# Performance work log

Hardware: AMD Instinct MI355X
Metric: run time of the kernel (lower is better)

Reference implementation:

```python
import jax, jax.numpy as jnp
import numpy as np

# SSD Detect post-processing constants (match init_kwargs)
NUM_CLASSES = 21
TOP_K = 200
CONF_THRESH = 0.95
NMS_THRESH = 0.45
M_CAND = 600      # candidate cap; chosen so all boxes passing CONF_THRESH fit (~437 expected)
NEG = -1e30


def setup_inputs() -> dict:
    key = jax.random.key(0)
    k1, k2, k3 = jax.random.split(key, 3)
    B, P, C = 8, 8732, NUM_CLASSES
    loc_data = jax.random.normal(k1, (B, P, 4), dtype=jnp.float32)
    conf_data = jax.random.uniform(k2, (B, P, C), dtype=jnp.float32)
    prior_data = jax.random.uniform(k3, (1, P, 4), dtype=jnp.float32)
    return {"loc_data": loc_data, "conf_data": conf_data, "prior_data": prior_data}


def _nms_lane(boxes_all, scores):
    """One (batch, class) lane. boxes_all: [P,4], scores: [P]. Returns [TOP_K, 5]."""
    pass_mask = scores > CONF_THRESH                       # [P]
    masked = jnp.where(pass_mask, scores, jnp.float32(NEG))
    vals, idx = jax.lax.top_k(masked, M_CAND)              # score-desc candidates (prior idx)
    valid = vals > jnp.float32(NEG / 2)                    # passed threshold
    cb = boxes_all[idx]                                    # [M,4] (x1,y1,x2,y2)
    x1, y1, x2, y2 = cb[:, 0], cb[:, 1], cb[:, 2], cb[:, 3]
    area = (x2 - x1) * (y2 - y1)                           # torchvision-style, no clamp
    xx1 = jnp.maximum(x1[:, None], x1[None, :])
    yy1 = jnp.maximum(y1[:, None], y1[None, :])
    xx2 = jnp.minimum(x2[:, None], x2[None, :])
    yy2 = jnp.minimum(y2[:, None], y2[None, :])
    inter = jnp.clip(xx2 - xx1, 0.0) * jnp.clip(yy2 - yy1, 0.0)
    iou = inter / (area[:, None] + area[None, :] - inter)  # [M,M]
    ar = jnp.arange(M_CAND)

    def body(i, supp):
        keep_i = valid[i] & jnp.logical_not(supp[i])
        return supp | (keep_i & (iou[i] > NMS_THRESH) & (ar > i))

    supp = jax.lax.fori_loop(0, M_CAND, body, jnp.zeros((M_CAND,), bool))
    keep = valid & jnp.logical_not(supp)
    order = jnp.argsort(jnp.logical_not(keep))             # stable: kept first, score order
    n = jnp.minimum(keep.sum(), TOP_K)                     # number of kept boxes (<= TOP_K)
    sel_prior = idx[order[:TOP_K]]                         # prior ids of kept (score order)
    slot_valid = jnp.arange(TOP_K) < n
    fp = jnp.argmax(pass_mask)                             # first prior passing threshold
    prior_ids = jnp.where(slot_valid, sel_prior, fp)       # pad with boxes[0] like torch
    out_scores = jnp.where(slot_valid, scores[prior_ids], 0.0)
    out = jnp.concatenate([out_scores[:, None], boxes_all[prior_ids]], axis=1)  # [K,5]
    return jnp.where(pass_mask.any(), out, jnp.zeros_like(out))


def _forward(loc_data, conf_data, prior_data):
    # prior_data is accepted per the torch signature but unused by the forward math.
    per_batch = jax.vmap(
        lambda boxes, conf_b: jax.vmap(lambda s: _nms_lane(boxes, s))(conf_b[:, 1:].T)
    )
    out_fg = per_batch(loc_data, conf_data)                # [B, C-1, K, 5]
    bg = jnp.zeros_like(out_fg[:, :1])                     # background class row stays 0
    return jnp.concatenate([bg, out_fg], axis=1)           # [B, C, K, 5]


def reference(loc_data, conf_data, prior_data):
    return _forward(loc_data, conf_data, prior_data)
```

## Files before the change

### kernel.cpp

```cpp
#include <hip/hip_runtime.h>
#include <float.h>
#include <math.h>


#define P_PRIORS  8732
#define C_CLASSES 21
#define B_BATCH   8
#define TOPK      200
#define MCAND     600
#define CONF_T    0.95f
#define NMS_T     0.45f
#define NB        64
#define MINB      0x3F733334u

__device__ __forceinline__ uint64_t pack_key(float sc, int p) {
    return ((uint64_t)__float_as_uint(sc) << 32) | (uint32_t)(~(uint32_t)p);
}
__device__ __forceinline__ int bucket_of(uint64_t key) {
    unsigned d = (unsigned)(key >> 32) - MINB;
    int b = (int)(d >> 14);
    return b < (NB - 1) ? b : (NB - 1);
}

#define IOU_ROW(BI, AI, MW, DIAG) do {                                   \
    float xx1 = fmaxf((BI).x, bj.x);                                     \
    float yy1 = fmaxf((BI).y, bj.y);                                     \
    float xx2 = fminf((BI).z, bj.z);                                     \
    float yy2 = fminf((BI).w, bj.w);                                     \
    float ww  = fmaxf(xx2 - xx1, 0.0f);                                  \
    float hh  = fmaxf(yy2 - yy1, 0.0f);                                  \
    float inter = ww * hh;                                               \
    float den   = ((AI) + aj) - inter;              \
    float iou   = inter / den;               \
    uint64_t m = __ballot(iou > NMS_T);                                  \
    if (k == c) m &= (DIAG);                                             \
    (MW) = (lid == k) ? m : (MW);                                        \
} while (0)

__device__ __forceinline__ void iou_chunk(
    int c, int wid, int lid, int M, int kend,
    const float4* s_jb, const float* s_area, uint64_t* s_bm)
{
    const int i0 = (c << 6) + wid;
    const float4 b0 = s_jb[i0],      b1 = s_jb[i0 + 16],
                 b2 = s_jb[i0 + 32], b3 = s_jb[i0 + 48];
    const float  a0 = s_area[i0],      a1 = s_area[i0 + 16],
                 a2 = s_area[i0 + 32], a3 = s_area[i0 + 48];
    const uint64_t d0 = ~0ull << (wid + 1);
    const uint64_t d1 = ~0ull << (wid + 17);
    const uint64_t d2 = ~0ull << (wid + 33);
    const uint64_t d3 = (wid == 15) ? 0ull : (~0ull << (wid + 49));
    uint64_t w0 = 0, w1 = 0, w2 = 0, w3 = 0;
    for (int k = c; k < kend; ++k) {
        const float4 bj = s_jb[(k << 6) + lid];
        const float  aj = s_area[(k << 6) + lid];
        IOU_ROW(b0, a0, w0, d0);
        IOU_ROW(b1, a1, w1, d1);
        IOU_ROW(b2, a2, w2, d2);
        IOU_ROW(b3, a3, w3, d3);
    }
    if (lid >= c && lid < kend) {
        if (i0      < M) s_bm[(size_t)(i0     ) * 10 + lid] = w0;
        if (i0 + 16 < M) s_bm[(size_t)(i0 + 16) * 10 + lid] = w1;
        if (i0 + 32 < M) s_bm[(size_t)(i0 + 32) * 10 + lid] = w2;
        if (i0 + 48 < M) s_bm[(size_t)(i0 + 48) * 10 + lid] = w3;
    }
}

__global__ __launch_bounds__(1024) void detect_one(
    const float* __restrict__ loc, const float* __restrict__ conf,
    float* __restrict__ out)
{
    const int b   = blockIdx.x & 7;
    const int cls = blockIdx.x >> 3;
    const int tid = threadIdx.x;
    float* o = out + ((size_t)(b * C_CLASSES + cls)) * TOPK * 5;

    if (cls == 0) {
        for (int k = tid; k < TOPK * 5; k += 1024) o[k] = 0.0f;
        return;
    }

    const float*  confb = conf + (size_t)b * P_PRIORS * C_CLASSES + cls;
    const float4* loc4  = (const float4*)(loc + (size_t)b * P_PRIORS * 4);

    __shared__ uint64_t s_bm[MCAND * 10];
    __shared__ float4   s_jb[640];
    __shared__ float    s_area[640];
    __shared__ float    s_ssc[MCAND];
    __shared__ int      s_bcnt[NB], s_bcur[NB], s_boff[NB];
    __shared__ int      s_cnt, s_fp;
    __shared__ uint64_t s_suppw[10], s_keepw[10];
    __shared__ int      s_prefix[10], s_n, s_mstop, s_done;

    uint64_t* s_k   = s_bm;
    uint64_t* s_g   = s_bm + 1024;
    uint64_t* s_srt = s_bm + 2048;

    if (tid < NB)                    s_bcnt[tid] = 0;
    else if (tid < 2 * NB)           s_bcur[tid - NB] = 0;
    else if (tid == 2 * NB)        { s_cnt = 0; s_fp = 0x7FFFFFFF; }
    __syncthreads();

    {
        const int lid = tid & 63;
        float vcur  = confb[(size_t)tid * C_CLASSES];
        float vnext = confb[(size_t)(tid + 1024) * C_CLASSES];
        #pragma unroll
        for (int r = 0; r < 9; ++r) {
            float v = vcur;
            vcur = vnext;
            if (r + 2 <= 7) {
                vnext = confb[(size_t)(tid + ((r + 2) << 10)) * C_CLASSES];
            } else if (r + 2 == 8) {
                int pn = tid + 8192;
                vnext = (pn < P_PRIORS) ? confb[(size_t)pn * C_CLASSES] : 0.0f;
            } else {
                vnext = 0.0f;
            }
            int p = tid + (r << 10);
            bool pass = v > CONF_T;
            uint64_t mask = __ballot(pass);
            if (mask != 0) {
                int leader = (int)__ffsll((unsigned long long)mask) - 1;
                int base = 0;
                if (lid == leader) {
                    base = atomicAdd(&s_cnt, __popcll(mask));
                    atomicMin(&s_fp, p);
                }
                base = __shfl(base, leader, 64);
                if (pass) {
                    int pos = base + __popcll(mask & ((1ull << lid) - 1ull));
                    if (pos < 1024) s_k[pos] = pack_key(v, p);
                }
            }
        }
    }
    __syncthreads();
    int cnt = s_cnt; if (cnt > 1024) cnt = 1024;
    if (cnt == 0) {
        for (int k = tid; k < TOPK * 5; k += 1024) o[k] = 0.0f;
        return;
    }

    for (int t = tid; t < cnt; t += 1024)
        atomicAdd(&s_bcnt[bucket_of(s_k[t])], 1);
    __syncthreads();

    if (tid < 64) {
        int c = s_bcnt[63 - tid];
        int incl = c;
        #pragma unroll
        for (int d = 1; d < 64; d <<= 1) {
            int u = __shfl_up(incl, d, 64);
            if (tid >= d) incl += u;
        }
        s_boff[63 - tid] = incl - c;
    }
    __syncthreads();

    for (int t = tid; t < cnt; t += 1024) {
        uint64_t kt = s_k[t];
        int bb = bucket_of(kt);
        s_g[s_boff[bb] + atomicAdd(&s_bcur[bb], 1)] = kt;
    }
    __syncthreads();

    const int M = cnt < MCAND ? cnt : MCAND;
    {
        const int wid = tid >> 6, lid = tid & 63;
        for (int bb = wid; bb < NB; bb += 16) {
            int st = s_boff[bb], n = s_bcnt[bb];
            for (int e = lid; e < n; e += 64) {
                uint64_t kq = s_g[st + e];
                int r = st;
                for (int q = 0; q < n; ++q)
                    r += (s_g[st + q] > kq) ? 1 : 0;
                if (r < MCAND) s_srt[r] = kq;
            }
        }
    }
    __syncthreads();

    for (int i = tid; i < M; i += 1024) {
        uint64_t key = s_srt[i];
        int p = (int)(~(uint32_t)key);
        s_ssc[i]  = __uint_as_float((uint32_t)(key >> 32));
        float4 bx = loc4[p];
        s_jb[i]   = bx;
        s_area[i] = (bx.z - bx.x) * (bx.w - bx.y);
    }
    for (int i = M + tid; i < 640; i += 1024) {
        s_jb[i]   = make_float4(INFINITY, INFINITY, INFINITY, INFINITY);
        s_area[i] = INFINITY;
    }
    const int fp = s_fp;
    __syncthreads();

    const int kmax = (M + 63) >> 6;
    const int kcap = kmax < 5 ? kmax : 5;

    {
        const int wid = tid >> 6, lid = tid & 63;
        const int w   = (lid < 10) ? lid : 0;
        uint64_t supp = 0;
        int kept = 0, mstop = M;
        const int nch = kcap;

        iou_chunk(0, wid, lid, M, kcap, s_jb, s_area, s_bm);
        __syncthreads();

        for (int c = 0; c < nch; ++c) {
            if (wid == 0) {
                const int ibeg = c << 6;
                const int iend = min(ibeg + 64, M);
                uint64_t rb[8];
                #pragma unroll
                for (int d = 0; d < 8; ++d) {
                    int i = ibeg + d;
                    rb[d] = (i < iend) ? s_bm[(size_t)i * 10 + w] : 0;
                }
                for (int i = ibeg; i < iend; ++i) {
                    uint64_t row = rb[i & 7];
                    if (w < c) row = 0;
                    int ip = i + 8;
                    rb[i & 7] = (ip < iend) ? s_bm[(size_t)ip * 10 + w] : 0;
                    bool mybit = (w == c) && ((supp >> (i & 63)) & 1ull);
                    if (!__any((int)mybit)) {
                        supp |= row;
                        if (++kept == TOPK) { mstop = i + 1; break; }
                    }
                }
                if (lid == 0) s_done = (kept >= TOPK) ? 1 : 0;
                if (kept < TOPK && c + 1 < nch)
                    iou_chunk(c + 1, 0, lid, M, kcap, s_jb, s_area, s_bm);
            } else if (c + 1 < nch) {
                iou_chunk(c + 1, wid, lid, M, kcap, s_jb, s_area, s_bm);
            }
            __syncthreads();
            if (s_done) break;
        }
        if (wid == 0) {
            if (lid < 10) s_suppw[lid] = supp;
            if (lid == 0) s_mstop = mstop;
        }
    }
    __syncthreads();

    if (s_done == 0 && M > 320) {
        const int wid = tid >> 6, lid = tid & 63;
        for (int i = wid; i < M; i += 16) {
            float4 bi = s_jb[i];
            float  ai = s_area[i];
            const int k0 = i >> 6;
            uint64_t diag = ((i & 63) == 63) ? 0ull : (~0ull << ((i & 63) + 1));
            uint64_t myw = 0;
            for (int k = k0; k < kmax; ++k) {
                float4 bj = s_jb[(k << 6) + lid];
                float  aj = s_area[(k << 6) + lid];
                float xx1 = fmaxf(bi.x, bj.x);
                float yy1 = fmaxf(bi.y, bj.y);
                float xx2 = fminf(bi.z, bj.z);
                float yy2 = fminf(bi.w, bj.w);
                float ww  = fmaxf(xx2 - xx1, 0.0f);
                float hh  = fmaxf(yy2 - yy1, 0.0f);
                float inter = ww * hh;
                float den   = (ai + aj) - inter;
                float iou   = inter / den;
                uint64_t m = __ballot(iou > NMS_T);
                if (k == k0) m &= diag;
                myw = (lid == k) ? m : myw;
            }
            if (lid >= k0 && lid < kmax) s_bm[(size_t)i * 10 + lid] = myw;
        }
        __syncthreads();
        if (tid < 64) {
            const int w = (tid < 10) ? tid : 0;
            uint64_t supp = 0;
            int kept = 0, ms = M;
            for (int i = 0; i < M; ++i) {
                uint64_t row = s_bm[(size_t)i * 10 + w];
                if (w < (i >> 6)) row = 0;
                unsigned part  = (unsigned)(supp >> (i & 32));
                unsigned wordv = (unsigned)__builtin_amdgcn_readlane((int)part, i >> 6);
                if (!((wordv >> (i & 31)) & 1u)) {
                    supp |= row;
                    if (++kept == TOPK) { ms = i + 1; break; }
                }
            }
            if (tid < 10) s_suppw[tid] = supp;
            if (tid == 0) s_mstop = ms;
        }
        __syncthreads();
    }

    if (tid == 0) {
        const int Me = s_mstop;
        int total = 0;
        for (int w = 0; w < 10; ++w) {
            uint64_t kw = 0;
            int rem = Me - (w << 6);
            if (rem > 0) {
                uint64_t vm = (rem >= 64) ? ~0ull : ((1ull << rem) - 1ull);
                kw = (~s_suppw[w]) & vm;
            }
            s_keepw[w]  = kw;
            s_prefix[w] = total;
            total += __popcll(kw);
        }
        s_n = total < TOPK ? total : TOPK;
    }
    __syncthreads();

    const int n  = s_n;
    const int Me = s_mstop;
    float4 fbox = loc4[fp];
    for (int k = tid; k < TOPK; k += 1024) {
        if (k >= n) {
            o[k * 5 + 0] = 0.0f;
            o[k * 5 + 1] = fbox.x; o[k * 5 + 2] = fbox.y;
            o[k * 5 + 3] = fbox.z; o[k * 5 + 4] = fbox.w;
        }
    }
    for (int t = tid; t < Me; t += 1024) {
        uint64_t kw = s_keepw[t >> 6];
        if ((kw >> (t & 63)) & 1ull) {
            int r = s_prefix[t >> 6] + __popcll(kw & ((1ull << (t & 63)) - 1ull));
            if (r < TOPK) {
                float4 bx = s_jb[t];
                o[r * 5 + 0] = s_ssc[t];
                o[r * 5 + 1] = bx.x; o[r * 5 + 2] = bx.y;
                o[r * 5 + 3] = bx.z; o[r * 5 + 4] = bx.w;
            }
        }
    }
}

extern "C" void kernel_launch(void* const* d_in, const int* in_sizes, int n_in,
                              void* d_out, int out_size, void* d_ws, size_t ws_size,
                              hipStream_t stream) {
    const float* loc  = (const float*)d_in[0];
    const float* conf = (const float*)d_in[1];
    float* out = (float*)d_out;
    (void)d_ws; (void)ws_size;

    detect_one<<<dim3(B_BATCH * C_CLASSES), dim3(1024), 0, stream>>>(loc, conf, out);
}
```

Before: 105.0 us.

## Replace bucketed rank sort with flat rank sort and prefetch IoU column boxes

Drops the 64-bucket histogram, scan and scatter stages and instead ranks each candidate key by comparing it against all candidates in a single O(n^2) pass over shared memory. This removes two barriers and the atomic bucket passes in exchange for more comparisons per thread (about 437 reads each, all threads reading the same address, which is a broadcast). It also software-pipelines the IoU chunk loop by loading the next column's box and area before computing the current rows, to hide LDS latency.

Measured after the change: 109.7 us. 4.5% more time.

```diff
diff --git a/kernel.cpp b/kernel.cpp
--- a/kernel.cpp
+++ b/kernel.cpp
@@ -10,16 +10,9 @@
 #define MCAND     600
 #define CONF_T    0.95f
 #define NMS_T     0.45f
-#define NB        64
-#define MINB      0x3F733334u
 
 __device__ __forceinline__ uint64_t pack_key(float sc, int p) {
     return ((uint64_t)__float_as_uint(sc) << 32) | (uint32_t)(~(uint32_t)p);
-}
-__device__ __forceinline__ int bucket_of(uint64_t key) {
-    unsigned d = (unsigned)(key >> 32) - MINB;
-    int b = (int)(d >> 14);
-    return b < (NB - 1) ? b : (NB - 1);
 }
 
 #define IOU_ROW(BI, AI, MW, DIAG) do {                                   \
@@ -51,13 +44,19 @@
     const uint64_t d2 = ~0ull << (wid + 33);
     const uint64_t d3 = (wid == 15) ? 0ull : (~0ull << (wid + 49));
     uint64_t w0 = 0, w1 = 0, w2 = 0, w3 = 0;
+    float4 bj = s_jb[(c << 6) + lid];
+    float  aj = s_area[(c << 6) + lid];
     for (int k = c; k < kend; ++k) {
-        const float4 bj = s_jb[(k << 6) + lid];
-        const float  aj = s_area[(k << 6) + lid];
+        float4 bjn = bj; float ajn = aj;
+        if (k + 1 < kend) {
+            bjn = s_jb[((k + 1) << 6) + lid];
+            ajn = s_area[((k + 1) << 6) + lid];
+        }
         IOU_ROW(b0, a0, w0, d0);
         IOU_ROW(b1, a1, w1, d1);
         IOU_ROW(b2, a2, w2, d2);
         IOU_ROW(b3, a3, w3, d3);
+        bj = bjn; aj = ajn;
     }
     if (lid >= c && lid < kend) {
         if (i0      < M) s_bm[(size_t)(i0     ) * 10 + lid] = w0;
@@ -88,18 +87,14 @@
     __shared__ float4   s_jb[640];
     __shared__ float    s_area[640];
     __shared__ float    s_ssc[MCAND];
-    __shared__ int      s_bcnt[NB], s_bcur[NB], s_boff[NB];
     __shared__ int      s_cnt, s_fp;
     __shared__ uint64_t s_suppw[10], s_keepw[10];
     __shared__ int      s_prefix[10], s_n, s_mstop, s_done;
 
     uint64_t* s_k   = s_bm;
-    uint64_t* s_g   = s_bm + 1024;
     uint64_t* s_srt = s_bm + 2048;
 
-    if (tid < NB)                    s_bcnt[tid] = 0;
-    else if (tid < 2 * NB)           s_bcur[tid - NB] = 0;
-    else if (tid == 2 * NB)        { s_cnt = 0; s_fp = 0x7FFFFFFF; }
+    if (tid == 0) { s_cnt = 0; s_fp = 0x7FFFFFFF; }
     __syncthreads();
 
     {
@@ -143,45 +138,16 @@
         return;
     }
 
-    for (int t = tid; t < cnt; t += 1024)
-        atomicAdd(&s_bcnt[bucket_of(s_k[t])], 1);
-    __syncthreads();
-
-    if (tid < 64) {
-        int c = s_bcnt[63 - tid];
-        int incl = c;
-        #pragma unroll
-        for (int d = 1; d < 64; d <<= 1) {
-            int u = __shfl_up(incl, d, 64);
-            if (tid >= d) incl += u;
-        }
-        s_boff[63 - tid] = incl - c;
-    }
-    __syncthreads();
-
     for (int t = tid; t < cnt; t += 1024) {
         uint64_t kt = s_k[t];
-        int bb = bucket_of(kt);
-        s_g[s_boff[bb] + atomicAdd(&s_bcur[bb], 1)] = kt;
+        int r = 0;
+        for (int q = 0; q < cnt; ++q)
+            r += (s_k[q] > kt) ? 1 : 0;
+        if (r < MCAND) s_srt[r] = kt;
     }
     __syncthreads();
 
     const int M = cnt < MCAND ? cnt : MCAND;
-    {
-        const int wid = tid >> 6, lid = tid & 63;
-        for (int bb = wid; bb < NB; bb += 16) {
-            int st = s_boff[bb], n = s_bcnt[bb];
-            for (int e = lid; e < n; e += 64) {
-                uint64_t kq = s_g[st + e];
-                int r = st;
-                for (int q = 0; q < n; ++q)
-                    r += (s_g[st + q] > kq) ? 1 : 0;
-                if (r < MCAND) s_srt[r] = kq;
-            }
-        }
-    }
-    __syncthreads();
-
     for (int i = tid; i < M; i += 1024) {
         uint64_t key = s_srt[i];
         int p = (int)(~(uint32_t)key);
```

## Offload next-chunk IoU rows from the NMS-scan wave to the other 15 waves

Applied to the files above, without the earlier changes.

Before, the IoU bitmask rows for each 64-candidate chunk were split across all 16 waves, so wave 0 had to finish its serial greedy NMS scan and then compute its own share of the next chunk. Now only waves 1-15 compute the rows, with some waves taking 5 rows instead of 4, and wave 0 does only the serial scan. This takes the IoU work off the critical path that wave 0 is on. In exchange the other waves carry more work and the extra fifth row is computed under a branch.

After: 103.8 us. Within noise of the previous version (-1.2%).

```diff
diff --git a/kernel.cpp b/kernel.cpp
--- a/kernel.cpp
+++ b/kernel.cpp
@@ -37,20 +37,25 @@
     (MW) = (lid == k) ? m : (MW);                                        \
 } while (0)
 
-__device__ __forceinline__ void iou_chunk(
-    int c, int wid, int lid, int M, int kend,
+__device__ __forceinline__ void iou_rows15(
+    int c, int w15, int lid, int M, int kend,
     const float4* s_jb, const float* s_area, uint64_t* s_bm)
 {
-    const int i0 = (c << 6) + wid;
-    const float4 b0 = s_jb[i0],      b1 = s_jb[i0 + 16],
-                 b2 = s_jb[i0 + 32], b3 = s_jb[i0 + 48];
-    const float  a0 = s_area[i0],      a1 = s_area[i0 + 16],
-                 a2 = s_area[i0 + 32], a3 = s_area[i0 + 48];
-    const uint64_t d0 = ~0ull << (wid + 1);
-    const uint64_t d1 = ~0ull << (wid + 17);
-    const uint64_t d2 = ~0ull << (wid + 33);
-    const uint64_t d3 = (wid == 15) ? 0ull : (~0ull << (wid + 49));
-    uint64_t w0 = 0, w1 = 0, w2 = 0, w3 = 0;
+    const int base = (c << 6);
+    const int r0 = base + (w15 - 1);
+    const int r1 = r0 + 15, r2 = r0 + 30, r3 = r0 + 45;
+    const bool has5 = (w15 <= 4);
+    const int r4 = base + 59 + w15;
+    const float4 b0 = s_jb[r0], b1 = s_jb[r1], b2 = s_jb[r2], b3 = s_jb[r3];
+    const float  a0 = s_area[r0], a1 = s_area[r1], a2 = s_area[r2], a3 = s_area[r3];
+    const float4 b4 = s_jb[has5 ? r4 : r0];
+    const float  a4 = s_area[has5 ? r4 : r0];
+    const uint64_t d0 = ~0ull << (w15);
+    const uint64_t d1 = ~0ull << (w15 + 15);
+    const uint64_t d2 = ~0ull << (w15 + 30);
+    const uint64_t d3 = ~0ull << (w15 + 45);
+    const uint64_t d4 = (59 + w15 == 63) ? 0ull : (~0ull << (60 + w15));
+    uint64_t w0 = 0, w1 = 0, w2 = 0, w3 = 0, w4 = 0;
     for (int k = c; k < kend; ++k) {
         const float4 bj = s_jb[(k << 6) + lid];
         const float  aj = s_area[(k << 6) + lid];
@@ -58,12 +63,14 @@
         IOU_ROW(b1, a1, w1, d1);
         IOU_ROW(b2, a2, w2, d2);
         IOU_ROW(b3, a3, w3, d3);
+        if (has5) { IOU_ROW(b4, a4, w4, d4); }
     }
     if (lid >= c && lid < kend) {
-        if (i0      < M) s_bm[(size_t)(i0     ) * 10 + lid] = w0;
-        if (i0 + 16 < M) s_bm[(size_t)(i0 + 16) * 10 + lid] = w1;
-        if (i0 + 32 < M) s_bm[(size_t)(i0 + 32) * 10 + lid] = w2;
-        if (i0 + 48 < M) s_bm[(size_t)(i0 + 48) * 10 + lid] = w3;
+        if (r0 < M) s_bm[(size_t)r0 * 10 + lid] = w0;
+        if (r1 < M) s_bm[(size_t)r1 * 10 + lid] = w1;
+        if (r2 < M) s_bm[(size_t)r2 * 10 + lid] = w2;
+        if (r3 < M) s_bm[(size_t)r3 * 10 + lid] = w3;
+        if (has5 && r4 < M) s_bm[(size_t)r4 * 10 + lid] = w4;
     }
 }
 
@@ -207,7 +214,7 @@
         int kept = 0, mstop = M;
         const int nch = kcap;
 
-        iou_chunk(0, wid, lid, M, kcap, s_jb, s_area, s_bm);
+        if (wid > 0) iou_rows15(0, wid, lid, M, kcap, s_jb, s_area, s_bm);
         __syncthreads();
 
         for (int c = 0; c < nch; ++c) {
@@ -232,10 +239,8 @@
                     }
                 }
                 if (lid == 0) s_done = (kept >= TOPK) ? 1 : 0;
-                if (kept < TOPK && c + 1 < nch)
-                    iou_chunk(c + 1, 0, lid, M, kcap, s_jb, s_area, s_bm);
             } else if (c + 1 < nch) {
-                iou_chunk(c + 1, wid, lid, M, kcap, s_jb, s_area, s_bm);
+                iou_rows15(c + 1, wid, lid, M, kcap, s_jb, s_area, s_bm);
             }
             __syncthreads();
             if (s_done) break;
```
